# Performance work log

Measured on AMD Instinct MI355X. Metric: run time of the kernel, lower is better.

Reference implementation:

```python
import jax, jax.numpy as jnp
import numpy as np

D_MODEL = 1024
NUM_HEADS = 16
D_K = D_MODEL // NUM_HEADS
B, S = 2, 2048


def setup_inputs() -> dict:
    key = jax.random.key(0)
    ks = jax.random.split(key, 11)
    sc = 1.0 / np.sqrt(D_MODEL)
    inp = {
        "query": jax.random.normal(ks[0], (B, S, D_MODEL), jnp.float32),
        "key": jax.random.normal(ks[1], (B, S, D_MODEL), jnp.float32),
        "value": jax.random.normal(ks[2], (B, S, D_MODEL), jnp.float32),
        "Wq": jax.random.normal(ks[3], (D_MODEL, D_MODEL), jnp.float32) * sc,
        "bq": jax.random.normal(ks[4], (D_MODEL,), jnp.float32) * sc,
        "Wk": jax.random.normal(ks[5], (D_MODEL, D_MODEL), jnp.float32) * sc,
        "bk": jax.random.normal(ks[6], (D_MODEL,), jnp.float32) * sc,
        "Wv": jax.random.normal(ks[7], (D_MODEL, D_MODEL), jnp.float32) * sc,
        "bv": jax.random.normal(ks[8], (D_MODEL,), jnp.float32) * sc,
        "Wo": jax.random.normal(ks[9], (D_MODEL, D_MODEL), jnp.float32) * sc,
        "bo": jax.random.normal(ks[10], (D_MODEL,), jnp.float32) * sc,
    }
    return inp


def reference(query, key, value, Wq, bq, Wk, bk, Wv, bv, Wo, bo):
    b = query.shape[0]
    # Linear projections (torch Linear: x @ W.T + b), W is [out, in]
    Q = query @ Wq.T + bq
    K = key @ Wk.T + bk
    V = value @ Wv.T + bv
    # [B, S, D] -> [B, H, S, d_k]
    Q = Q.reshape(b, -1, NUM_HEADS, D_K).transpose(0, 2, 1, 3)
    K = K.reshape(b, -1, NUM_HEADS, D_K).transpose(0, 2, 1, 3)
    V = V.reshape(b, -1, NUM_HEADS, D_K).transpose(0, 2, 1, 3)
    # Scaled dot-product attention (mask=None, dropout inactive in eval)
    scores = jnp.einsum("bhqd,bhkd->bhqk", Q, K) / jnp.sqrt(jnp.float32(D_K))
    attn = jax.nn.softmax(scores, axis=-1)
    out = jnp.einsum("bhqk,bhkd->bhqd", attn, V)
    # [B, H, S, d_k] -> [B, S, D]
    out = out.transpose(0, 2, 1, 3).reshape(b, -1, D_MODEL)
    return out @ Wo.T + bo
```

## Files before the change

### kernel.cpp

```cpp
#include <hip/hip_runtime.h>

typedef __bf16 bf16x8 __attribute__((ext_vector_type(8)));
typedef __bf16 bf16x4 __attribute__((ext_vector_type(4)));
typedef float f32x4 __attribute__((ext_vector_type(4)));

#define D_MODEL 1024
#define NUM_HEADS 16
#define DK 64
#define BATCH 2
#define SEQ 2048
#define M_ROWS (BATCH*SEQ)

#define QSCALE 0.18033688011112042f

#if defined(__has_builtin)
#if __has_builtin(__builtin_amdgcn_exp2f)
#define EXP2(x) __builtin_amdgcn_exp2f(x)
#endif
#endif
#ifndef EXP2
#define EXP2(x) exp2f(x)
#endif

#define GLOAD_LDS16(gp, lp) __builtin_amdgcn_global_load_lds( \
    (__attribute__((address_space(1))) void*)(gp), \
    (__attribute__((address_space(3))) void*)(lp), 16, 0, 0)

#define ACT ((size_t)M_ROWS * D_MODEL)
#define WSZ ((size_t)D_MODEL * D_MODEL)

__global__ __launch_bounds__(256) void cvt_all(
    const float* __restrict__ q, const float* __restrict__ k,
    const float* __restrict__ v, const float* __restrict__ wq,
    const float* __restrict__ wk, const float* __restrict__ wv,
    const float* __restrict__ wo, __bf16* __restrict__ dst)
{
  size_t e = ((size_t)blockIdx.x * 256 + threadIdx.x) * 8;
  const float* s;
  size_t off;
  if (e < 3 * ACT) {
    int t = (int)(e >> 22);
    s = t == 0 ? q : (t == 1 ? k : v);
    off = e & (ACT - 1);
  } else {
    size_t e2 = e - 3 * ACT;
    int t = (int)(e2 >> 20);
    s = t == 0 ? wq : (t == 1 ? wk : (t == 2 ? wv : wo));
    off = e2 & (WSZ - 1);
  }
  float4 a = *(const float4*)(s + off);
  float4 b = *(const float4*)(s + off + 4);
  bf16x8 o;
  o[0] = (__bf16)a.x; o[1] = (__bf16)a.y; o[2] = (__bf16)a.z; o[3] = (__bf16)a.w;
  o[4] = (__bf16)b.x; o[5] = (__bf16)b.y; o[6] = (__bf16)b.z; o[7] = (__bf16)b.w;
  *(bf16x8*)(dst + e) = o;
}

template <typename OutT>
__device__ __forceinline__ void gemm_body(
    const __bf16* __restrict__ A, const __bf16* __restrict__ W,
    const float* __restrict__ bias, OutT* __restrict__ C,
    int M, int N, int K, int m0, int n0, float scale)
{
  __shared__ __align__(16) __bf16 sA[2][128*64];
  __shared__ __align__(16) __bf16 sB[2][64*64];
  const int tid  = threadIdx.x;
  const int wave = tid >> 6;
  const int lane = tid & 63;
  const int l16  = lane & 15;
  const int quad = lane >> 4;
  const int wm = (wave >> 1) * 64;
  const int wn = (wave & 1) * 32;

  f32x4 acc[4][2] = {};

  const int gsw = (((tid & 7) ^ ((tid >> 3) & 7))) * 8;
  long aoff[4], boff[2];
#pragma unroll
  for (int i = 0; i < 4; i++) {
    int row = (i * 256 + tid) >> 3;
    aoff[i] = (long)(m0 + row) * K + gsw;
  }
#pragma unroll
  for (int i = 0; i < 2; i++) {
    int row = (i * 256 + tid) >> 3;
    boff[i] = (long)(n0 + row) * K + gsw;
  }
  const int rsw = l16 & 7;

  const int NT = K / 64;

#pragma unroll
  for (int i = 0; i < 4; i++)
    GLOAD_LDS16(A + aoff[i], (char*)sA[0] + i * 4096 + tid * 16);
#pragma unroll
  for (int i = 0; i < 2; i++)
    GLOAD_LDS16(W + boff[i], (char*)sB[0] + i * 4096 + tid * 16);
  __syncthreads();

  for (int t = 0; t < NT; t++) {
    const __bf16* sAc = sA[t & 1];
    const __bf16* sBc = sB[t & 1];
    if (t + 1 < NT) {
      int k1 = (t + 1) * 64;
      char* sAn = (char*)sA[(t + 1) & 1];
      char* sBn = (char*)sB[(t + 1) & 1];
#pragma unroll
      for (int i = 0; i < 4; i++)
        GLOAD_LDS16(A + aoff[i] + k1, sAn + i * 4096 + tid * 16);
#pragma unroll
      for (int i = 0; i < 2; i++)
        GLOAD_LDS16(W + boff[i] + k1, sBn + i * 4096 + tid * 16);
    }
#pragma unroll
    for (int ks = 0; ks < 2; ks++) {
      bf16x8 af[4], bf[2];
#pragma unroll
      for (int i = 0; i < 4; i++)
        af[i] = *(const bf16x8*)&sAc[(wm + i * 16 + l16) * 64 + ((ks * 4 + quad) ^ rsw) * 8];
#pragma unroll
      for (int j = 0; j < 2; j++)
        bf[j] = *(const bf16x8*)&sBc[(wn + j * 16 + l16) * 64 + ((ks * 4 + quad) ^ rsw) * 8];
#pragma unroll
      for (int i = 0; i < 4; i++)
#pragma unroll
        for (int j = 0; j < 2; j++)
          acc[i][j] = __builtin_amdgcn_mfma_f32_16x16x32_bf16(af[i], bf[j], acc[i][j], 0, 0, 0);
    }
    if (t + 1 < NT) __syncthreads();
  }

#pragma unroll
  for (int j = 0; j < 2; j++) {
    int col = n0 + wn + j * 16 + l16;
    float bv = bias[col];
#pragma unroll
    for (int i = 0; i < 4; i++) {
      long row0 = m0 + wm + i * 16 + quad * 4;
#pragma unroll
      for (int r = 0; r < 4; r++)
        C[(row0 + r) * N + col] = (OutT)((acc[i][j][r] + bv) * scale);
    }
  }
}

__global__ __launch_bounds__(256) void gemm_qkv(
    const __bf16* __restrict__ Abase, const __bf16* __restrict__ Wbase,
    const float* __restrict__ b0, const float* __restrict__ b1,
    const float* __restrict__ b2, __bf16* __restrict__ Cbase)
{
  int lid = blockIdx.x + (blockIdx.y << 4) + (blockIdx.z << 9);
  int swz = (lid & 7) * 192 + (lid >> 3);
  int x = swz & 15, y = (swz >> 4) & 31, z = swz >> 9;
  const __bf16* A = Abase + (size_t)z * M_ROWS * D_MODEL;
  const __bf16* W = Wbase + (size_t)z * D_MODEL * D_MODEL;
  const float* bias = z == 0 ? b0 : (z == 1 ? b1 : b2);
  float scale = z == 0 ? QSCALE : 1.0f;
  __bf16* C = Cbase + (size_t)z * M_ROWS * D_MODEL;
  gemm_body<__bf16>(A, W, bias, C, M_ROWS, D_MODEL, D_MODEL,
                    y * 128, x * 64, scale);
}

__global__ __launch_bounds__(256) void gemm_out(
    const __bf16* __restrict__ A, const __bf16* __restrict__ W,
    const float* __restrict__ bias, float* __restrict__ C)
{
  int lid = blockIdx.x + (blockIdx.y << 4);
  int swz = (lid & 7) * 64 + (lid >> 3);
  int x = swz & 15, y = swz >> 4;
  gemm_body<float>(A, W, bias, C, M_ROWS, D_MODEL, D_MODEL,
                   y * 128, x * 64, 1.0f);
}

__global__ __launch_bounds__(512) void attn_kernel(
    const __bf16* __restrict__ Q, const __bf16* __restrict__ K,
    const __bf16* __restrict__ V, __bf16* __restrict__ O)
{
  constexpr int SV_LD = 136;

  __shared__ __align__(16) __bf16 sK[128 * 64];
  __shared__ __align__(16) __bf16 sVt[DK * SV_LD];
  __shared__ float lsbuf[8][16];

  const int tid  = threadIdx.x;
  const int wave = tid >> 6;
  const int g    = wave & 3;
  const int kh   = wave >> 2;
  const int lane = tid & 63;
  const int l16  = lane & 15;
  const int quad = lane >> 4;

  const int bh = blockIdx.y;
  const int b  = bh >> 4, h = bh & (NUM_HEADS - 1);
  const int q0 = blockIdx.x * 64;
  const long base = (long)b * SEQ * D_MODEL + h * DK;

  const __bf16* qrow = Q + base + (long)(q0 + g * 16 + l16) * D_MODEL + quad * 8;
  const bf16x8 aq0 = *(const bf16x8*)(qrow);
  const bf16x8 aq1 = *(const bf16x8*)(qrow + 32);

  const int gsw = (((tid & 7) ^ ((tid >> 3) & 7))) * 8;
  const __bf16* kp[2];
#pragma unroll
  for (int i = 0; i < 2; i++)
    kp[i] = K + base + (long)((i * 512 + tid) >> 3) * D_MODEL + gsw;
  const int rsw = l16 & 7;

  const __bf16* vp0 = V + base + (long)(2 * lane) * D_MODEL + wave * 8;
  const int k5 = (2 * lane) & 31;
  const int pos5 = ((k5 & 12) << 1) | ((k5 & 16) >> 2) | (k5 & 3);
  const int vcol = (lane >> 4) * 16 + (pos5 >> 1);

  uint4 kr0 = *(const uint4*)(kp[0]);
  uint4 kr1 = *(const uint4*)(kp[1]);
  uint4 vr0 = *(const uint4*)(vp0);
  uint4 vr1 = *(const uint4*)(vp0 + D_MODEL);

  f32x4 lacc = {};
  f32x4 o[4] = {};

  for (int t = 0; t < SEQ / 128; t++) {
    __syncthreads();
    *(uint4*)((char*)sK + tid * 16) = kr0;
    *(uint4*)((char*)sK + 8192 + tid * 16) = kr1;
    {
      const ushort* e0 = (const ushort*)&vr0;
      const ushort* e1 = (const ushort*)&vr1;
      uint* dst = (uint*)sVt;
#pragma unroll
      for (int j = 0; j < 8; j++)
        dst[(wave * 8 + j) * (SV_LD / 2) + vcol] = (uint)e0[j] | ((uint)e1[j] << 16);
    }
    if (t + 1 < SEQ / 128) {
      long adv = (long)(t + 1) * 128 * D_MODEL;
      kr0 = *(const uint4*)(kp[0] + adv);
      kr1 = *(const uint4*)(kp[1] + adv);
      vr0 = *(const uint4*)(vp0 + adv);
      vr1 = *(const uint4*)(vp0 + adv + D_MODEL);
    }
    __syncthreads();

#pragma unroll
    for (int kl = 0; kl < 2; kl++) {
      const int kt = kh * 2 + kl;
      bf16x8 af;
#pragma unroll
      for (int hh = 0; hh < 2; hh++) {
        int nt = kt * 2 + hh;
        bf16x8 b0 = *(const bf16x8*)&sK[(nt * 16 + l16) * 64 + (quad ^ rsw) * 8];
        bf16x8 b1 = *(const bf16x8*)&sK[(nt * 16 + l16) * 64 + ((4 + quad) ^ rsw) * 8];
        f32x4 z = {};
        __builtin_amdgcn_s_setprio(1);
        z = __builtin_amdgcn_mfma_f32_16x16x32_bf16(b0, aq0, z, 0, 0, 0);
        z = __builtin_amdgcn_mfma_f32_16x16x32_bf16(b1, aq1, z, 0, 0, 0);
        __builtin_amdgcn_s_setprio(0);
        f32x4 p;
#pragma unroll
        for (int r = 0; r < 4; r++) p[r] = EXP2(z[r]);
        lacc += p;
#pragma unroll
        for (int r = 0; r < 4; r++) af[hh * 4 + r] = (__bf16)p[r];
      }
      __builtin_amdgcn_s_setprio(1);
#pragma unroll
      for (int dt = 0; dt < 4; dt++) {
        bf16x8 bv = *(const bf16x8*)&sVt[(dt * 16 + l16) * SV_LD + kt * 32 + quad * 8];
        o[dt] = __builtin_amdgcn_mfma_f32_16x16x32_bf16(af, bv, o[dt], 0, 0, 0);
      }
      __builtin_amdgcn_s_setprio(0);
    }
  }

  float ls = lacc[0] + lacc[1] + lacc[2] + lacc[3];
  ls += __shfl_xor(ls, 16, 64);
  ls += __shfl_xor(ls, 32, 64);

  __syncthreads();
  if (quad == 0) lsbuf[wave][l16] = ls;
  f32x4* scr = (f32x4*)sK;
  if (kh == 1) {
#pragma unroll
    for (int dt = 0; dt < 4; dt++)
      scr[dt * 256 + g * 64 + lane] = o[dt];
  }
  __syncthreads();
  if (kh == 0) {
    float lst = lsbuf[g][l16] + lsbuf[4 + g][l16];
    float rls[4];
#pragma unroll
    for (int r = 0; r < 4; r++)
      rls[r] = 1.0f / __shfl(lst, quad * 4 + r, 64);
#pragma unroll
    for (int dt = 0; dt < 4; dt++) {
      f32x4 oo = o[dt] + scr[dt * 256 + g * 64 + lane];
#pragma unroll
      for (int r = 0; r < 4; r++) {
        int s = q0 + g * 16 + quad * 4 + r;
        int d = dt * 16 + l16;
        O[base + (long)s * D_MODEL + d] = (__bf16)(oo[r] * rls[r]);
      }
    }
  }
}

extern "C" void kernel_launch(void* const* d_in, const int* in_sizes, int n_in,
                              void* d_out, int out_size, void* d_ws, size_t ws_size,
                              hipStream_t stream) {
  const float* q  = (const float*)d_in[0];
  const float* k  = (const float*)d_in[1];
  const float* v  = (const float*)d_in[2];
  const float* Wq = (const float*)d_in[3];
  const float* bq = (const float*)d_in[4];
  const float* Wk = (const float*)d_in[5];
  const float* bk = (const float*)d_in[6];
  const float* Wv = (const float*)d_in[7];
  const float* bv = (const float*)d_in[8];
  const float* Wo = (const float*)d_in[9];
  const float* bo = (const float*)d_in[10];
  float* out = (float*)d_out;

  __bf16* qc  = (__bf16*)d_ws;
  __bf16* Wqc = qc + 3 * ACT;
  __bf16* wsQ = Wqc + 4 * WSZ;
  __bf16* wsAo = qc;

  dim3 blk(256);
  cvt_all<<<dim3((3 * ACT + 4 * WSZ) / 2048), blk, 0, stream>>>(
      q, k, v, Wq, Wk, Wv, Wo, qc);

  gemm_qkv<<<dim3(D_MODEL / 64, M_ROWS / 128, 3), blk, 0, stream>>>(
      qc, Wqc, bq, bk, bv, wsQ);

  attn_kernel<<<dim3(SEQ / 64, BATCH * NUM_HEADS), dim3(512), 0, stream>>>(
      wsQ, wsQ + ACT, wsQ + 2 * ACT, wsAo);

  gemm_out<<<dim3(D_MODEL / 64, M_ROWS / 128), blk, 0, stream>>>(
      wsAo, Wqc + 3 * WSZ, bo, out);
}
```

Baseline: 228.4 us.

## Split-K the output projection GEMM with atomic accumulation

```diff
diff --git a/kernel.cpp b/kernel.cpp
--- a/kernel.cpp
+++ b/kernel.cpp
@@ -56,11 +56,11 @@
   *(bf16x8*)(dst + e) = o;
 }
 
-template <typename OutT>
+template <typename OutT, bool ATOMIC>
 __device__ __forceinline__ void gemm_body(
     const __bf16* __restrict__ A, const __bf16* __restrict__ W,
     const float* __restrict__ bias, OutT* __restrict__ C,
-    int M, int N, int K, int m0, int n0, float scale)
+    int N, int Kstride, int KLEN, int m0, int n0, float scale)
 {
   __shared__ __align__(16) __bf16 sA[2][128*64];
   __shared__ __align__(16) __bf16 sB[2][64*64];
@@ -79,16 +79,16 @@
 #pragma unroll
   for (int i = 0; i < 4; i++) {
     int row = (i * 256 + tid) >> 3;
-    aoff[i] = (long)(m0 + row) * K + gsw;
+    aoff[i] = (long)(m0 + row) * Kstride + gsw;
   }
 #pragma unroll
   for (int i = 0; i < 2; i++) {
     int row = (i * 256 + tid) >> 3;
-    boff[i] = (long)(n0 + row) * K + gsw;
+    boff[i] = (long)(n0 + row) * Kstride + gsw;
   }
   const int rsw = l16 & 7;
 
-  const int NT = K / 64;
+  const int NT = KLEN / 64;
 
 #pragma unroll
   for (int i = 0; i < 4; i++)
@@ -133,13 +133,16 @@
 #pragma unroll
   for (int j = 0; j < 2; j++) {
     int col = n0 + wn + j * 16 + l16;
-    float bv = bias[col];
+    float bv = bias ? bias[col] : 0.0f;
 #pragma unroll
     for (int i = 0; i < 4; i++) {
       long row0 = m0 + wm + i * 16 + quad * 4;
 #pragma unroll
-      for (int r = 0; r < 4; r++)
-        C[(row0 + r) * N + col] = (OutT)((acc[i][j][r] + bv) * scale);
+      for (int r = 0; r < 4; r++) {
+        float v = (acc[i][j][r] + bv) * scale;
+        if (ATOMIC) atomicAdd((float*)&C[(row0 + r) * N + col], v);
+        else        C[(row0 + r) * N + col] = (OutT)v;
+      }
     }
   }
 }
@@ -157,19 +160,20 @@
   const float* bias = z == 0 ? b0 : (z == 1 ? b1 : b2);
   float scale = z == 0 ? QSCALE : 1.0f;
   __bf16* C = Cbase + (size_t)z * M_ROWS * D_MODEL;
-  gemm_body<__bf16>(A, W, bias, C, M_ROWS, D_MODEL, D_MODEL,
-                    y * 128, x * 64, scale);
+  gemm_body<__bf16, false>(A, W, bias, C, D_MODEL, D_MODEL, D_MODEL,
+                           y * 128, x * 64, scale);
 }
 
 __global__ __launch_bounds__(256) void gemm_out(
     const __bf16* __restrict__ A, const __bf16* __restrict__ W,
     const float* __restrict__ bias, float* __restrict__ C)
 {
-  int lid = blockIdx.x + (blockIdx.y << 4);
-  int swz = (lid & 7) * 64 + (lid >> 3);
-  int x = swz & 15, y = swz >> 4;
-  gemm_body<float>(A, W, bias, C, M_ROWS, D_MODEL, D_MODEL,
-                   y * 128, x * 64, 1.0f);
+  int lid = blockIdx.x + (blockIdx.y << 4) + (blockIdx.z << 9);
+  int swz = (lid & 7) * 128 + (lid >> 3);
+  int x = swz & 15, y = (swz >> 4) & 31, z = swz >> 9;
+  gemm_body<float, true>(A + z * 512, W + z * 512,
+                         z == 0 ? bias : nullptr, C,
+                         D_MODEL, D_MODEL, 512, y * 128, x * 64, 1.0f);
 }
 
 __global__ __launch_bounds__(512) void attn_kernel(
@@ -324,6 +328,8 @@
   __bf16* wsQ = Wqc + 4 * WSZ;
   __bf16* wsAo = qc;
 
+  hipMemsetAsync(out, 0, (size_t)M_ROWS * D_MODEL * sizeof(float), stream);
+
   dim3 blk(256);
   cvt_all<<<dim3((3 * ACT + 4 * WSZ) / 2048), blk, 0, stream>>>(
       q, k, v, Wq, Wk, Wv, Wo, qc);
@@ -334,6 +340,6 @@
   attn_kernel<<<dim3(SEQ / 64, BATCH * NUM_HEADS), dim3(512), 0, stream>>>(
       wsQ, wsQ + ACT, wsQ + 2 * ACT, wsAo);
 
-  gemm_out<<<dim3(D_MODEL / 64, M_ROWS / 128), blk, 0, stream>>>(
+  gemm_out<<<dim3(16, 32, 2), blk, 0, stream>>>(
       wsAo, Wqc + 3 * WSZ, bo, out);
 }
```

New measurement: 256.1 us. 1.12x slower.

## Remap attention waves to two query tiles each, splitting keys four ways

Applied to the files above, without the earlier changes.

```diff
diff --git a/kernel.cpp b/kernel.cpp
--- a/kernel.cpp
+++ b/kernel.cpp
@@ -180,12 +180,12 @@
 
   __shared__ __align__(16) __bf16 sK[128 * 64];
   __shared__ __align__(16) __bf16 sVt[DK * SV_LD];
-  __shared__ float lsbuf[8][16];
+  __shared__ float lsbuf[8][2][16];
 
   const int tid  = threadIdx.x;
   const int wave = tid >> 6;
-  const int g    = wave & 3;
-  const int kh   = wave >> 2;
+  const int qp   = wave & 1;
+  const int kh   = wave >> 1;
   const int lane = tid & 63;
   const int l16  = lane & 15;
   const int quad = lane >> 4;
@@ -195,9 +195,12 @@
   const int q0 = blockIdx.x * 64;
   const long base = (long)b * SEQ * D_MODEL + h * DK;
 
-  const __bf16* qrow = Q + base + (long)(q0 + g * 16 + l16) * D_MODEL + quad * 8;
-  const bf16x8 aq0 = *(const bf16x8*)(qrow);
-  const bf16x8 aq1 = *(const bf16x8*)(qrow + 32);
+  const __bf16* qrow0 = Q + base + (long)(q0 + qp * 32 + l16) * D_MODEL + quad * 8;
+  const __bf16* qrow1 = qrow0 + (long)16 * D_MODEL;
+  const bf16x8 aq00 = *(const bf16x8*)(qrow0);
+  const bf16x8 aq01 = *(const bf16x8*)(qrow0 + 32);
+  const bf16x8 aq10 = *(const bf16x8*)(qrow1);
+  const bf16x8 aq11 = *(const bf16x8*)(qrow1 + 32);
 
   const int gsw = (((tid & 7) ^ ((tid >> 3) & 7))) * 8;
   const __bf16* kp[2];
@@ -216,8 +219,8 @@
   uint4 vr0 = *(const uint4*)(vp0);
   uint4 vr1 = *(const uint4*)(vp0 + D_MODEL);
 
-  f32x4 lacc = {};
-  f32x4 o[4] = {};
+  f32x4 lacc0 = {}, lacc1 = {};
+  f32x4 o0[4] = {}, o1[4] = {};
 
   for (int t = 0; t < SEQ / 128; t++) {
     __syncthreads();
@@ -240,64 +243,98 @@
     }
     __syncthreads();
 
-#pragma unroll
-    for (int kl = 0; kl < 2; kl++) {
-      const int kt = kh * 2 + kl;
-      bf16x8 af;
-#pragma unroll
-      for (int hh = 0; hh < 2; hh++) {
-        int nt = kt * 2 + hh;
-        bf16x8 b0 = *(const bf16x8*)&sK[(nt * 16 + l16) * 64 + (quad ^ rsw) * 8];
-        bf16x8 b1 = *(const bf16x8*)&sK[(nt * 16 + l16) * 64 + ((4 + quad) ^ rsw) * 8];
-        f32x4 z = {};
-        __builtin_amdgcn_s_setprio(1);
-        z = __builtin_amdgcn_mfma_f32_16x16x32_bf16(b0, aq0, z, 0, 0, 0);
-        z = __builtin_amdgcn_mfma_f32_16x16x32_bf16(b1, aq1, z, 0, 0, 0);
-        __builtin_amdgcn_s_setprio(0);
-        f32x4 p;
-#pragma unroll
-        for (int r = 0; r < 4; r++) p[r] = EXP2(z[r]);
-        lacc += p;
-#pragma unroll
-        for (int r = 0; r < 4; r++) af[hh * 4 + r] = (__bf16)p[r];
-      }
+    const int kt = kh;
+    bf16x8 af0, af1;
+#pragma unroll
+    for (int hh = 0; hh < 2; hh++) {
+      int nt = kt * 2 + hh;
+      bf16x8 b0 = *(const bf16x8*)&sK[(nt * 16 + l16) * 64 + (quad ^ rsw) * 8];
+      bf16x8 b1 = *(const bf16x8*)&sK[(nt * 16 + l16) * 64 + ((4 + quad) ^ rsw) * 8];
+      f32x4 z0 = {}, z1 = {};
       __builtin_amdgcn_s_setprio(1);
-#pragma unroll
-      for (int dt = 0; dt < 4; dt++) {
-        bf16x8 bv = *(const bf16x8*)&sVt[(dt * 16 + l16) * SV_LD + kt * 32 + quad * 8];
-        o[dt] = __builtin_amdgcn_mfma_f32_16x16x32_bf16(af, bv, o[dt], 0, 0, 0);
-      }
+      z0 = __builtin_amdgcn_mfma_f32_16x16x32_bf16(b0, aq00, z0, 0, 0, 0);
+      z0 = __builtin_amdgcn_mfma_f32_16x16x32_bf16(b1, aq01, z0, 0, 0, 0);
+      z1 = __builtin_amdgcn_mfma_f32_16x16x32_bf16(b0, aq10, z1, 0, 0, 0);
+      z1 = __builtin_amdgcn_mfma_f32_16x16x32_bf16(b1, aq11, z1, 0, 0, 0);
       __builtin_amdgcn_s_setprio(0);
-    }
-  }
-
-  float ls = lacc[0] + lacc[1] + lacc[2] + lacc[3];
-  ls += __shfl_xor(ls, 16, 64);
-  ls += __shfl_xor(ls, 32, 64);
-
-  __syncthreads();
-  if (quad == 0) lsbuf[wave][l16] = ls;
+      f32x4 p0, p1;
+#pragma unroll
+      for (int r = 0; r < 4; r++) p0[r] = EXP2(z0[r]);
+#pragma unroll
+      for (int r = 0; r < 4; r++) p1[r] = EXP2(z1[r]);
+      lacc0 += p0;
+      lacc1 += p1;
+#pragma unroll
+      for (int r = 0; r < 4; r++) af0[hh * 4 + r] = (__bf16)p0[r];
+#pragma unroll
+      for (int r = 0; r < 4; r++) af1[hh * 4 + r] = (__bf16)p1[r];
+    }
+    __builtin_amdgcn_s_setprio(1);
+#pragma unroll
+    for (int dt = 0; dt < 4; dt++) {
+      bf16x8 bv = *(const bf16x8*)&sVt[(dt * 16 + l16) * SV_LD + kt * 32 + quad * 8];
+      o0[dt] = __builtin_amdgcn_mfma_f32_16x16x32_bf16(af0, bv, o0[dt], 0, 0, 0);
+      o1[dt] = __builtin_amdgcn_mfma_f32_16x16x32_bf16(af1, bv, o1[dt], 0, 0, 0);
+    }
+    __builtin_amdgcn_s_setprio(0);
+  }
+
+  float ls0 = lacc0[0] + lacc0[1] + lacc0[2] + lacc0[3];
+  ls0 += __shfl_xor(ls0, 16, 64);
+  ls0 += __shfl_xor(ls0, 32, 64);
+  float ls1 = lacc1[0] + lacc1[1] + lacc1[2] + lacc1[3];
+  ls1 += __shfl_xor(ls1, 16, 64);
+  ls1 += __shfl_xor(ls1, 32, 64);
+
+  __syncthreads();
   f32x4* scr = (f32x4*)sK;
+  const int sbase = qp * 8 * 64;
+  if (quad == 0) { lsbuf[wave][0][l16] = ls0; lsbuf[wave][1][l16] = ls1; }
+  if (kh == 3) {
+#pragma unroll
+    for (int dt = 0; dt < 4; dt++) {
+      scr[sbase + dt * 64 + lane] = o0[dt];
+      scr[sbase + (4 + dt) * 64 + lane] = o1[dt];
+    }
+  }
+  __syncthreads();
+  if (kh == 2) {
+#pragma unroll
+    for (int dt = 0; dt < 4; dt++) {
+      scr[sbase + dt * 64 + lane] += o0[dt];
+      scr[sbase + (4 + dt) * 64 + lane] += o1[dt];
+    }
+  }
+  __syncthreads();
   if (kh == 1) {
 #pragma unroll
-    for (int dt = 0; dt < 4; dt++)
-      scr[dt * 256 + g * 64 + lane] = o[dt];
+    for (int dt = 0; dt < 4; dt++) {
+      scr[sbase + dt * 64 + lane] += o0[dt];
+      scr[sbase + (4 + dt) * 64 + lane] += o1[dt];
+    }
   }
   __syncthreads();
   if (kh == 0) {
-    float lst = lsbuf[g][l16] + lsbuf[4 + g][l16];
-    float rls[4];
-#pragma unroll
-    for (int r = 0; r < 4; r++)
-      rls[r] = 1.0f / __shfl(lst, quad * 4 + r, 64);
-#pragma unroll
-    for (int dt = 0; dt < 4; dt++) {
-      f32x4 oo = o[dt] + scr[dt * 256 + g * 64 + lane];
+    float lt0 = lsbuf[qp][0][l16] + lsbuf[2 + qp][0][l16] +
+                lsbuf[4 + qp][0][l16] + lsbuf[6 + qp][0][l16];
+    float lt1 = lsbuf[qp][1][l16] + lsbuf[2 + qp][1][l16] +
+                lsbuf[4 + qp][1][l16] + lsbuf[6 + qp][1][l16];
+    float rls0[4], rls1[4];
+#pragma unroll
+    for (int r = 0; r < 4; r++) {
+      rls0[r] = 1.0f / __shfl(lt0, quad * 4 + r, 64);
+      rls1[r] = 1.0f / __shfl(lt1, quad * 4 + r, 64);
+    }
+#pragma unroll
+    for (int dt = 0; dt < 4; dt++) {
+      f32x4 a0 = o0[dt] + scr[sbase + dt * 64 + lane];
+      f32x4 a1 = o1[dt] + scr[sbase + (4 + dt) * 64 + lane];
 #pragma unroll
       for (int r = 0; r < 4; r++) {
-        int s = q0 + g * 16 + quad * 4 + r;
+        int s = q0 + qp * 32 + quad * 4 + r;
         int d = dt * 16 + l16;
-        O[base + (long)s * D_MODEL + d] = (__bf16)(oo[r] * rls[r]);
+        O[base + (long)s * D_MODEL + d] = (__bf16)(a0[r] * rls0[r]);
+        O[base + (long)(s + 16) * D_MODEL + d] = (__bf16)(a1[r] * rls1[r]);
       }
     }
   }
```

New measurement: 255.5 us. +11.8%, slower.
